# Kernel tuning notes

Measured on AMD Instinct MI355X. Metric: run time of the kernel, lower is better.

## Reference

```python
import jax, jax.numpy as jnp
import numpy as np

HIDDEN = 384
NDIM = 3
N_POINTS = 100000
N_SUPER = 2048
MAX_DEG = 32
RADIUS = 0.045
INPUT_DIM = 3


def _sincos_embed(coords):
    # ContinuousSincosEmbed: dim=384, ndim=3 -> 128 channels per spatial dim (64 sin + 64 cos)
    eff = HIDDEN // NDIM  # 128
    omega = jnp.arange(0, eff, 2, dtype=jnp.float32) / eff
    freq = 1.0 / (10000.0 ** omega)  # [eff//2]
    out = coords[..., None] * freq  # [..., ndim, eff//2]
    emb = jnp.concatenate([jnp.sin(out), jnp.cos(out)], axis=-1)  # [..., ndim, eff]
    return emb.reshape(coords.shape[:-1] + (HIDDEN,))


def _radius_neighbors(pos, sn_idx):
    # numpy preprocessing equivalent of torch_geometric.nn.pool.radius with
    # max_num_neighbors=MAX_DEG; fixed-size padded [S, K] output + validity mask.
    nbr = np.zeros((N_SUPER, MAX_DEG), np.int32)
    mask = np.zeros((N_SUPER, MAX_DEG), bool)
    pos2 = (pos ** 2).sum(-1)
    r2 = RADIUS * RADIUS
    chunk = 128
    for i0 in range(0, N_SUPER, chunk):
        sp = pos[sn_idx[i0:i0 + chunk]]
        d2 = (sp ** 2).sum(-1)[:, None] + pos2[None, :] - 2.0 * (sp @ pos.T)
        within = d2 <= r2
        for j in range(sp.shape[0]):
            idx = np.nonzero(within[j])[0][:MAX_DEG]
            nbr[i0 + j, :len(idx)] = idx
            mask[i0 + j, :len(idx)] = True
    return nbr, mask


def setup_inputs() -> dict:
    rng = np.random.default_rng(0)
    pos = rng.random((N_POINTS, NDIM)).astype(np.float32)
    sn_idx = np.sort(rng.choice(N_POINTS, N_SUPER, replace=False)).astype(np.int32)
    nbr, mask = _radius_neighbors(pos, sn_idx)
    key = jax.random.key(0)
    ks = jax.random.split(key, 6)
    s = 0.02  # truncnormal002 init scale
    return {
        "input_pos": jnp.asarray(pos),
        "input_feat": jax.random.normal(ks[0], (N_POINTS, INPUT_DIM), jnp.float32),
        "supernode_idx": jnp.asarray(sn_idx),
        "neighbor_idx": jnp.asarray(nbr),
        "neighbor_mask": jnp.asarray(mask),
        "W_in": jax.random.normal(ks[1], (INPUT_DIM, HIDDEN), jnp.float32) * s,
        "b_in": jnp.zeros((HIDDEN,), jnp.float32),
        "W1": jax.random.normal(ks[2], (2 * HIDDEN, HIDDEN), jnp.float32) * s,
        "b1": jnp.zeros((HIDDEN,), jnp.float32),
        "W2": jax.random.normal(ks[3], (HIDDEN, HIDDEN), jnp.float32) * s,
        "b2": jnp.zeros((HIDDEN,), jnp.float32),
        "W_proj": jax.random.normal(ks[4], (2 * HIDDEN, HIDDEN), jnp.float32) * s,
        "b_proj": jnp.zeros((HIDDEN,), jnp.float32),
    }


def reference(input_pos, input_feat, supernode_idx, neighbor_idx, neighbor_mask,
              W_in, b_in, W1, b1, W2, b2, W_proj, b_proj):
    # point embeddings: continuous sincos pos embed + input feature projection
    x = _sincos_embed(input_pos) + input_feat @ W_in + b_in          # [N, D]
    sn = x[supernode_idx]                                            # [S, D] supernode pos embed
    src = x[neighbor_idx]                                            # [S, K, D] gathered neighbors
    dst = jnp.broadcast_to(sn[:, None, :], src.shape)                # [S, K, D]
    h = jnp.concatenate([src, dst], axis=-1)                         # [S, K, 2D]
    # message MLP (Linear -> GELU(exact) -> Linear), as nn.GELU default
    h = jax.nn.gelu(h @ W1 + b1, approximate=False) @ W2 + b2        # [S, K, D]
    # masked mean == segment_csr(..., reduce='mean') over variable-degree edges
    m = neighbor_mask[..., None].astype(h.dtype)
    agg = (h * m).sum(axis=1) / jnp.maximum(m.sum(axis=1), 1.0)      # [S, D]
    # readd_supernode_pos: concat supernode pos embed, project 2D -> D
    out = jnp.concatenate([agg, sn], axis=-1) @ W_proj + b_proj      # [S, D]
    return out[None]                                                 # [1, S, D] (batch_size=1)
```

## Files before the change

### kernel.cpp

```cpp
#include <hip/hip_runtime.h>
#include <hip/hip_bf16.h>
#include <cstdint>

#define HIDDEN 384
#define NSUPER 2048
#define MAXDEG 32
#define FRAGS (12*24*64)
#define WBLK  (FRAGS*8)

typedef __attribute__((ext_vector_type(8))) short bf16x8;
typedef __attribute__((ext_vector_type(4))) float f32x4;

#define SWZ(row, col) ((col) ^ (((row)&7)<<3))

__device__ inline unsigned short f2bf(float f) {
    __hip_bfloat16 h = __float2bfloat16(f);
    return *reinterpret_cast<unsigned short*>(&h);
}
__device__ inline bf16x8 pack8(const float* v) {
    union { bf16x8 v8; unsigned short u[8]; } u;
    #pragma unroll
    for (int i = 0; i < 8; ++i) u.u[i] = f2bf(v[i]);
    return u.v8;
}
__device__ inline float fast_erf(float x) {
    float ax = fabsf(x);
    float t  = 1.0f / fmaf(0.3275911f, ax, 1.0f);
    float p  = t*(0.254829592f + t*(-0.284496736f + t*(1.421413741f +
               t*(-1.453152027f + t*1.061405429f))));
    float e  = __expf(-ax*ax);
    return copysignf(1.0f - p*e, x);
}
__device__ inline float gelu(float y) {
    return 0.5f * y * (1.0f + fast_erf(y * 0.70710678118654752f));
}

__global__ __launch_bounds__(256)
void prep(const float* __restrict__ W1, const float* __restrict__ W2,
          const float* __restrict__ Wp, const unsigned int* __restrict__ mask,
          unsigned short* __restrict__ w1sf, unsigned short* __restrict__ w1df,
          unsigned short* __restrict__ w2f,  unsigned short* __restrict__ wpf,
          int* __restrict__ flag) {
    const int b = blockIdx.x;
    if (b == 360) {
        __shared__ int s;
        if (threadIdx.x == 0) s = 0;
        __syncthreads();
        int bad = 0;
        for (int i = threadIdx.x; i < 16384; i += 256)
            if (mask[i] > 1u) bad = 1;
        if (bad) s = 1;
        __syncthreads();
        if (threadIdx.x == 0) *flag = s;
        return;
    }
    const int grp = b / 72, sub = b % 72;
    const float* W; unsigned short* out;
    switch (grp) {
        case 0: W = W1;              out = w1sf; break;
        case 1: W = W1 + 384*HIDDEN; out = w1df; break;
        case 2: W = W2;              out = w2f;  break;
        case 3: W = Wp;              out = wpf;  break;
        default:W = Wp + 384*HIDDEN; out = wpf + WBLK; break;
    }
    const int idx = sub * 256 + threadIdx.x;
    const int l   = idx & 63;
    const int frag= idx >> 6;
    const int nt  = frag % 24;
    const int kt  = frag / 24;
    const int col = nt * 16 + (l & 15);
    const int k0  = kt * 32 + (l >> 4) * 8;
    unsigned int pk[4];
    #pragma unroll
    for (int j = 0; j < 4; ++j) {
        unsigned int lo = f2bf(W[(k0 + 2*j)     * HIDDEN + col]);
        unsigned int hi = f2bf(W[(k0 + 2*j + 1) * HIDDEN + col]);
        pk[j] = lo | (hi << 16);
    }
    *reinterpret_cast<uint4*>(&out[(size_t)idx * 8]) =
        *reinterpret_cast<const uint4*>(pk);
}

__global__ __launch_bounds__(256)
void k_embdst(const float* __restrict__ pos, const float* __restrict__ feat,
              const int* __restrict__ sn_idx,
              const float* __restrict__ W_in, const float* __restrict__ b_in,
              const unsigned short* __restrict__ W1df, const float* __restrict__ b1,
              unsigned short* __restrict__ snxb, float* __restrict__ dstv)
{
    __shared__ unsigned short E[64][384];
    __shared__ float WINT[HIDDEN][4];
    __shared__ float PF[64][8];
    __shared__ float FREQ[64];

    const int rg = blockIdx.x >> 1, ch = blockIdx.x & 1;
    const int t  = threadIdx.x;

    if (t < 64) {
        const int pi = sn_idx[rg*64 + t];
        PF[t][0]=pos[pi*3];  PF[t][1]=pos[pi*3+1];  PF[t][2]=pos[pi*3+2];
        PF[t][3]=feat[pi*3]; PF[t][4]=feat[pi*3+1]; PF[t][5]=feat[pi*3+2];
        FREQ[t] = exp2f(-(float)t * 0.2076205059304601f);
    }
    for (int d = t; d < HIDDEN; d += 256) {
        WINT[d][0]=W_in[d]; WINT[d][1]=W_in[HIDDEN+d];
        WINT[d][2]=W_in[2*HIDDEN+d]; WINT[d][3]=b_in[d];
    }
    __syncthreads();

    const int er = t >> 2, seg = t & 3;
    #pragma unroll
    for (int blk = 0; blk < 12; ++blk) {
        const int dim0 = blk*32 + seg*8;
        float v[8];
        #pragma unroll
        for (int i = 0; i < 8; ++i) {
            const int dim = dim0 + i;
            const int cc  = dim >> 7;
            const float a = PF[er][cc] * FREQ[dim & 63];
            const float base = ((dim >> 6) & 1) ? __cosf(a) : __sinf(a);
            const float4 wv = *(const float4*)WINT[dim];
            v[i] = base + PF[er][3]*wv.x + PF[er][4]*wv.y + PF[er][5]*wv.z + wv.w;
        }
        const bf16x8 pk = pack8(v);
        *(bf16x8*)&E[er][SWZ(er, dim0)] = pk;
        if (ch == 0)
            *(bf16x8*)&snxb[(size_t)(rg*64 + er)*HIDDEN + dim0] = pk;
    }
    __syncthreads();

    const int w = t>>6, l = t&63, lg = l>>4, l15 = l&15;
    const int wgm = w>>1, wgn = w&1;
    f32x4 acc[2][6];
    #pragma unroll
    for (int mt=0; mt<2; ++mt)
        #pragma unroll
        for (int nt=0; nt<6; ++nt) acc[mt][nt] = (f32x4){0.f,0.f,0.f,0.f};
    const int ntb = (ch*2 + wgn) * 6;
    for (int kt = 0; kt < 12; ++kt) {
        bf16x8 a[2], bfr[6];
        const unsigned short* bp = &W1df[((size_t)(kt*24 + ntb)*64 + l)*8];
        #pragma unroll
        for (int nt=0; nt<6; ++nt) bfr[nt] = *(const bf16x8*)(bp + (size_t)nt*512);
        #pragma unroll
        for (int mt=0; mt<2; ++mt)
            a[mt] = *(const bf16x8*)&E[wgm*32 + mt*16 + l15][SWZ(l15, kt*32 + lg*8)];
        #pragma unroll
        for (int mt=0; mt<2; ++mt)
            #pragma unroll
            for (int nt=0; nt<6; ++nt)
                acc[mt][nt] = __builtin_amdgcn_mfma_f32_16x16x32_bf16(a[mt], bfr[nt], acc[mt][nt], 0,0,0);
    }
    #pragma unroll
    for (int mt=0; mt<2; ++mt)
        #pragma unroll
        for (int nt=0; nt<6; ++nt) {
            const int col = ch*192 + wgn*96 + nt*16 + l15;
            #pragma unroll
            for (int r=0; r<4; ++r) {
                const int row = rg*64 + wgm*32 + mt*16 + lg*4 + r;
                dstv[(size_t)row*HIDDEN + col] = acc[mt][nt][r] + b1[col];
            }
        }
}

__global__ __launch_bounds__(256, 2)
void k_mlp(const float* __restrict__ pos, const float* __restrict__ feat,
           const int* __restrict__ nbr_idx, const void* __restrict__ mask_raw,
           const int* __restrict__ mask_fmt,
           const float* __restrict__ W_in, const float* __restrict__ b_in,
           const float* __restrict__ dstv,
           const unsigned short* __restrict__ W1f,
           const unsigned short* __restrict__ W2f,
           const float* __restrict__ b2, unsigned short* __restrict__ aggb)
{
    __shared__ unsigned short G[4*12*64*8];
    __shared__ float WINT[HIDDEN][4];
    __shared__ float DSTV[2][HIDDEN];
    __shared__ float PF[64][8];
    __shared__ float CNT[2];

    const int t  = threadIdx.x;
    const int bm = blockIdx.x;

    if (t < 64) {
        const int e  = bm*64 + t;
        const int pi = nbr_idx[e];
        PF[t][0]=pos[pi*3];  PF[t][1]=pos[pi*3+1];  PF[t][2]=pos[pi*3+2];
        PF[t][3]=feat[pi*3]; PF[t][4]=feat[pi*3+1]; PF[t][5]=feat[pi*3+2];
        const int fmt = *mask_fmt;
        const int mv  = fmt ? (int)((const unsigned char*)mask_raw)[e]
                            : ((const int*)mask_raw)[e];
        PF[t][6] = mv ? 1.0f : 0.0f;
    }
    for (int d = t; d < HIDDEN; d += 256) {
        WINT[d][0]=W_in[d]; WINT[d][1]=W_in[HIDDEN+d];
        WINT[d][2]=W_in[2*HIDDEN+d]; WINT[d][3]=b_in[d];
    }
    for (int i = t; i < 2*HIDDEN; i += 256)
        ((float*)DSTV)[i] = dstv[(size_t)bm*2*HIDDEN + i];
    __syncthreads();
    if (t < 2) {
        float c = 0.f;
        for (int s = 0; s < 32; ++s) c += PF[t*32+s][6];
        CNT[t] = c;
    }

    {
        const int er = t >> 2, seg = t & 3;
        float frA[8], frB[8];
        #pragma unroll
        for (int i = 0; i < 8; ++i) {
            frA[i] = exp2f(-(float)(seg*8 + i)      * 0.2076205059304601f);
            frB[i] = exp2f(-(float)(32 + seg*8 + i) * 0.2076205059304601f);
        }
        const float f0 = PF[er][3], f1 = PF[er][4], f2 = PF[er][5];
        const int slotbase = (er>>4)*12*64 + seg*16 + (er&15);
        #pragma unroll
        for (int blk = 0; blk < 12; ++blk) {
            const float pc = PF[er][blk>>2];
            float v[8];
            #pragma unroll
            for (int i = 0; i < 8; ++i) {
                const int dim = blk*32 + seg*8 + i;
                const float fr = (blk & 1) ? frB[i] : frA[i];
                const float a  = pc * fr;
                const float base = ((blk>>1) & 1) ? __cosf(a) : __sinf(a);
                const float4 wv = *(const float4*)WINT[dim];
                v[i] = fmaf(f0, wv.x, fmaf(f1, wv.y, fmaf(f2, wv.z, base + wv.w)));
            }
            *(bf16x8*)&G[(size_t)(slotbase + blk*64)*8] = pack8(v);
        }
    }
    __syncthreads();

    const int l = t & 63, ng = t >> 6, lg = l >> 4, l15 = l & 15;

    f32x4 acc[4][6];
    bf16x8 bA[6], bB[6];

    #define LOADB(dst, Wf, kt)                                                  \
        { const unsigned short* bp_ = &Wf[((size_t)((kt)*24 + ng*6)*64 + l)*8]; \
          _Pragma("unroll")                                                     \
          for (int nt_ = 0; nt_ < 6; ++nt_)                                     \
              dst[nt_] = *(const bf16x8*)(bp_ + (size_t)nt_*512); }
    #define AREAD(a_, kt)                                                       \
        { _Pragma("unroll")                                                     \
          for (int mt_ = 0; mt_ < 4; ++mt_)                                     \
              a_[mt_] = *(const bf16x8*)&G[(size_t)(((mt_*12 + (kt))*64) + l)*8]; }
    #define MFMA6(bfr, a_)                                                      \
        { _Pragma("unroll")                                                     \
          for (int mt_ = 0; mt_ < 4; ++mt_)                                     \
              _Pragma("unroll")                                                 \
              for (int nt_ = 0; nt_ < 6; ++nt_)                                 \
                  acc[mt_][nt_] = __builtin_amdgcn_mfma_f32_16x16x32_bf16(      \
                      a_[mt_], bfr[nt_], acc[mt_][nt_], 0, 0, 0); }

    #pragma unroll
    for (int mt=0; mt<4; ++mt)
        #pragma unroll
        for (int nt=0; nt<6; ++nt) acc[mt][nt] = (f32x4){0.f,0.f,0.f,0.f};
    LOADB(bA, W1f, 0); LOADB(bB, W1f, 1);
    #pragma unroll
    for (int kt = 0; kt < 12; kt += 2) {
        bf16x8 a[4];
        AREAD(a, kt);
        MFMA6(bA, a);
        if (kt + 2 < 12) LOADB(bA, W1f, kt + 2);
        AREAD(a, kt + 1);
        MFMA6(bB, a);
        if (kt + 3 < 12) LOADB(bB, W1f, kt + 3);
    }
    __syncthreads();

    #pragma unroll
    for (int mt=0; mt<4; ++mt) {
        const int sl = mt >> 1;
        #pragma unroll
        for (int nt=0; nt<6; ++nt) {
            const int col = ng*96 + nt*16 + l15;
            const float dv = DSTV[sl][col];
            const int base = ((mt*12 + (col>>5))*64 + ((col>>3)&3)*16 + lg*4)*8 + (col&7);
            #pragma unroll
            for (int r=0; r<4; ++r)
                G[base + r*8] = f2bf(gelu(acc[mt][nt][r] + dv));
        }
    }
    __syncthreads();

    #pragma unroll
    for (int mt=0; mt<4; ++mt)
        #pragma unroll
        for (int nt=0; nt<6; ++nt) acc[mt][nt] = (f32x4){0.f,0.f,0.f,0.f};
    LOADB(bA, W2f, 0); LOADB(bB, W2f, 1);
    #pragma unroll
    for (int kt = 0; kt < 12; kt += 2) {
        bf16x8 a[4];
        AREAD(a, kt);
        MFMA6(bA, a);
        if (kt + 2 < 12) LOADB(bA, W2f, kt + 2);
        AREAD(a, kt + 1);
        MFMA6(bB, a);
        if (kt + 3 < 12) LOADB(bB, W2f, kt + 3);
    }

    #pragma unroll
    for (int nt=0; nt<6; ++nt) {
        const int col = ng*96 + nt*16 + l15;
        float s0 = 0.f, s1 = 0.f;
        #pragma unroll
        for (int mt=0; mt<4; ++mt) {
            float p = 0.f;
            #pragma unroll
            for (int r=0; r<4; ++r)
                p += PF[mt*16 + lg*4 + r][6] * acc[mt][nt][r];
            if (mt < 2) s0 += p; else s1 += p;
        }
        s0 += __shfl_xor(s0,16); s0 += __shfl_xor(s0,32);
        s1 += __shfl_xor(s1,16); s1 += __shfl_xor(s1,32);
        if (lg == 0) {
            const float bb = b2[col];
            const int sn0 = bm*2;
            const float c0 = CNT[0], c1 = CNT[1];
            aggb[(size_t)sn0*HIDDEN + col]     = f2bf(s0 / fmaxf(c0,1.f) + bb*(c0>0.f?1.f:0.f));
            aggb[(size_t)(sn0+1)*HIDDEN + col] = f2bf(s1 / fmaxf(c1,1.f) + bb*(c1>0.f?1.f:0.f));
        }
    }
    #undef LOADB
    #undef AREAD
    #undef MFMA6
}

__global__ __launch_bounds__(256)
void k_proj(const unsigned short* __restrict__ aggb,
            const unsigned short* __restrict__ snxb,
            const unsigned short* __restrict__ wpf,
            const float* __restrict__ bp, float* __restrict__ out) {
    const int rg = blockIdx.x >> 2, cq = blockIdx.x & 3;
    const int t = threadIdx.x, w = t>>6, l = t&63, lg = l>>4, l15 = l&15;
    const int wgm = w>>1, wgn = w&1;
    const int r0 = rg*64 + wgm*32;
    const int ntb = cq*6 + wgn*3;
    f32x4 acc[2][3];
    #pragma unroll
    for (int mt=0; mt<2; ++mt)
        #pragma unroll
        for (int nt=0; nt<3; ++nt) acc[mt][nt] = (f32x4){0.f,0.f,0.f,0.f};
    #pragma unroll 2
    for (int kt = 0; kt < 24; ++kt) {
        const unsigned short* Ab = (kt < 12) ? aggb : snxb;
        const unsigned short* Wb = (kt < 12) ? wpf  : wpf + WBLK;
        const int ktt = (kt < 12) ? kt : kt - 12;
        bf16x8 a[2], bfr[3];
        const unsigned short* bpp = &Wb[((size_t)(ktt*24 + ntb)*64 + l)*8];
        #pragma unroll
        for (int nt=0; nt<3; ++nt) bfr[nt] = *(const bf16x8*)(bpp + (size_t)nt*512);
        #pragma unroll
        for (int mt=0; mt<2; ++mt)
            a[mt] = *(const bf16x8*)&Ab[(size_t)(r0 + mt*16 + l15)*HIDDEN + ktt*32 + lg*8];
        #pragma unroll
        for (int mt=0; mt<2; ++mt)
            #pragma unroll
            for (int nt=0; nt<3; ++nt)
                acc[mt][nt] = __builtin_amdgcn_mfma_f32_16x16x32_bf16(a[mt], bfr[nt], acc[mt][nt], 0,0,0);
    }
    #pragma unroll
    for (int mt=0; mt<2; ++mt)
        #pragma unroll
        for (int nt=0; nt<3; ++nt) {
            const int col = cq*96 + wgn*48 + nt*16 + l15;
            #pragma unroll
            for (int r=0; r<4; ++r) {
                const int row = r0 + mt*16 + lg*4 + r;
                out[(size_t)row*HIDDEN + col] = acc[mt][nt][r] + bp[col];
            }
        }
}

extern "C" void kernel_launch(void* const* d_in, const int* in_sizes, int n_in,
                              void* d_out, int out_size, void* d_ws, size_t ws_size,
                              hipStream_t stream) {
    const float* pos   = (const float*)d_in[0];
    const float* feat  = (const float*)d_in[1];
    const int*   sn    = (const int*)d_in[2];
    const int*   nbr   = (const int*)d_in[3];
    const void*  mask  = d_in[4];
    const float* W_in  = (const float*)d_in[5];
    const float* b_in  = (const float*)d_in[6];
    const float* W1    = (const float*)d_in[7];
    const float* b1    = (const float*)d_in[8];
    const float* W2    = (const float*)d_in[9];
    const float* b2    = (const float*)d_in[10];
    const float* Wp    = (const float*)d_in[11];
    const float* bpv   = (const float*)d_in[12];
    float* out = (float*)d_out;

    char* base = (char*)d_ws;
    int* flag = (int*)base;
    unsigned short* w1sf = (unsigned short*)(base + 256);
    unsigned short* w1df = w1sf + WBLK;
    unsigned short* w2f  = w1df + WBLK;
    unsigned short* wpf  = w2f  + WBLK;
    unsigned short* snxb = wpf  + 2*(size_t)WBLK;
    unsigned short* aggb = snxb + (size_t)NSUPER*HIDDEN;
    float* dstv = (float*)(aggb + (size_t)NSUPER*HIDDEN);

    hipLaunchKernelGGL(prep, dim3(361), dim3(256), 0, stream,
                       W1, W2, Wp, (const unsigned int*)mask, w1sf, w1df, w2f, wpf, flag);
    hipLaunchKernelGGL(k_embdst, dim3(64), dim3(256), 0, stream,
                       pos, feat, sn, W_in, b_in, w1df, b1, snxb, dstv);
    hipLaunchKernelGGL(k_mlp, dim3(1024), dim3(256), 0, stream,
                       pos, feat, nbr, mask, flag, W_in, b_in, dstv, w1sf, w2f, b2, aggb);
    hipLaunchKernelGGL(k_proj, dim3(128), dim3(256), 0, stream,
                       aggb, snxb, wpf, bpv, out);
}
```

Measured before the change: 94.98 us.

## Fold supernode embedding into prep, split dst GEMM, raise k_mlp occupancy

Supernode embedding computation moves into extra blocks of the prep kernel, and the dst-side W1 GEMM becomes a separate k_dstv kernel. That kernel reads the bf16 embedding from global memory and uses 128 smaller blocks instead of 64. In k_mlp, the first weight fragments are prefetched before the embedding phase, dstv values are held in registers instead of shared memory, and W_in is stored in shared memory as bf16 to cut LDS use. k_mlp also computes sin/cos once per frequency pair, raises the occupancy target to 3 blocks per CU, and raises wave priority around MFMA bursts. Risks are register spills at the higher occupancy target and a small precision loss from the bf16 W_in.

```diff
diff --git a/kernel.cpp b/kernel.cpp
--- a/kernel.cpp
+++ b/kernel.cpp
@@ -11,11 +11,12 @@
 typedef __attribute__((ext_vector_type(8))) short bf16x8;
 typedef __attribute__((ext_vector_type(4))) float f32x4;
 
-#define SWZ(row, col) ((col) ^ (((row)&7)<<3))
-
 __device__ inline unsigned short f2bf(float f) {
     __hip_bfloat16 h = __float2bfloat16(f);
     return *reinterpret_cast<unsigned short*>(&h);
+}
+__device__ inline float b2f(unsigned short s) {
+    return __uint_as_float(((unsigned int)s) << 16);
 }
 __device__ inline bf16x8 pack8(const float* v) {
     union { bf16x8 v8; unsigned short u[8]; } u;
@@ -38,20 +39,71 @@
 __global__ __launch_bounds__(256)
 void prep(const float* __restrict__ W1, const float* __restrict__ W2,
           const float* __restrict__ Wp, const unsigned int* __restrict__ mask,
+          const float* __restrict__ pos, const float* __restrict__ feat,
+          const int* __restrict__ sn_idx,
+          const float* __restrict__ W_in, const float* __restrict__ b_in,
           unsigned short* __restrict__ w1sf, unsigned short* __restrict__ w1df,
           unsigned short* __restrict__ w2f,  unsigned short* __restrict__ wpf,
-          int* __restrict__ flag) {
+          unsigned short* __restrict__ snxb, int* __restrict__ flag) {
     const int b = blockIdx.x;
+    const int t = threadIdx.x;
     if (b == 360) {
         __shared__ int s;
-        if (threadIdx.x == 0) s = 0;
+        if (t == 0) s = 0;
         __syncthreads();
         int bad = 0;
-        for (int i = threadIdx.x; i < 16384; i += 256)
+        for (int i = t; i < 16384; i += 256)
             if (mask[i] > 1u) bad = 1;
         if (bad) s = 1;
         __syncthreads();
-        if (threadIdx.x == 0) *flag = s;
+        if (t == 0) *flag = s;
+        return;
+    }
+    if (b > 360) {
+        __shared__ float W4[HIDDEN][4];
+        __shared__ float P6[64][7];
+        const int eb = b - 361;
+        if (t < 64) {
+            const int pi = sn_idx[eb*64 + t];
+            P6[t][0]=pos[pi*3];  P6[t][1]=pos[pi*3+1];  P6[t][2]=pos[pi*3+2];
+            P6[t][3]=feat[pi*3]; P6[t][4]=feat[pi*3+1]; P6[t][5]=feat[pi*3+2];
+        }
+        for (int d = t; d < HIDDEN; d += 256) {
+            W4[d][0]=W_in[d]; W4[d][1]=W_in[HIDDEN+d];
+            W4[d][2]=W_in[2*HIDDEN+d]; W4[d][3]=b_in[d];
+        }
+        __syncthreads();
+        const int er = t >> 2, seg = t & 3;
+        float frA[8], frB[8];
+        #pragma unroll
+        for (int i = 0; i < 8; ++i) {
+            frA[i] = exp2f(-(float)(seg*8 + i)      * 0.2076205059304601f);
+            frB[i] = exp2f(-(float)(32 + seg*8 + i) * 0.2076205059304601f);
+        }
+        const float f0 = P6[er][3], f1 = P6[er][4], f2 = P6[er][5];
+        #pragma unroll
+        for (int cc = 0; cc < 3; ++cc) {
+            const float pc = P6[er][cc];
+            float sL[8], sH[8], cL[8], cH[8];
+            #pragma unroll
+            for (int i = 0; i < 8; ++i) {
+                const float aL = pc*frA[i], aH = pc*frB[i];
+                sL[i]=__sinf(aL); sH[i]=__sinf(aH); cL[i]=__cosf(aL); cH[i]=__cosf(aH);
+            }
+            #pragma unroll
+            for (int q = 0; q < 4; ++q) {
+                const float* bb = (q==0)?sL:(q==1)?sH:(q==2)?cL:cH;
+                const int blk = cc*4 + q;
+                float v[8];
+                #pragma unroll
+                for (int i = 0; i < 8; ++i) {
+                    const int dim = blk*32 + seg*8 + i;
+                    const float4 wv = *(const float4*)W4[dim];
+                    v[i] = fmaf(f0, wv.x, fmaf(f1, wv.y, fmaf(f2, wv.z, bb[i] + wv.w)));
+                }
+                *(bf16x8*)&snxb[(size_t)(eb*64 + er)*HIDDEN + blk*32 + seg*8] = pack8(v);
+            }
+        }
         return;
     }
     const int grp = b / 72, sub = b % 72;
@@ -63,7 +115,7 @@
         case 3: W = Wp;              out = wpf;  break;
         default:W = Wp + 384*HIDDEN; out = wpf + WBLK; break;
     }
-    const int idx = sub * 256 + threadIdx.x;
+    const int idx = sub * 256 + t;
     const int l   = idx & 63;
     const int frag= idx >> 6;
     const int nt  = frag % 24;
@@ -82,89 +134,48 @@
 }
 
 __global__ __launch_bounds__(256)
-void k_embdst(const float* __restrict__ pos, const float* __restrict__ feat,
-              const int* __restrict__ sn_idx,
-              const float* __restrict__ W_in, const float* __restrict__ b_in,
-              const unsigned short* __restrict__ W1df, const float* __restrict__ b1,
-              unsigned short* __restrict__ snxb, float* __restrict__ dstv)
-{
-    __shared__ unsigned short E[64][384];
-    __shared__ float WINT[HIDDEN][4];
-    __shared__ float PF[64][8];
-    __shared__ float FREQ[64];
-
-    const int rg = blockIdx.x >> 1, ch = blockIdx.x & 1;
-    const int t  = threadIdx.x;
-
-    if (t < 64) {
-        const int pi = sn_idx[rg*64 + t];
-        PF[t][0]=pos[pi*3];  PF[t][1]=pos[pi*3+1];  PF[t][2]=pos[pi*3+2];
-        PF[t][3]=feat[pi*3]; PF[t][4]=feat[pi*3+1]; PF[t][5]=feat[pi*3+2];
-        FREQ[t] = exp2f(-(float)t * 0.2076205059304601f);
-    }
-    for (int d = t; d < HIDDEN; d += 256) {
-        WINT[d][0]=W_in[d]; WINT[d][1]=W_in[HIDDEN+d];
-        WINT[d][2]=W_in[2*HIDDEN+d]; WINT[d][3]=b_in[d];
-    }
-    __syncthreads();
-
-    const int er = t >> 2, seg = t & 3;
-    #pragma unroll
-    for (int blk = 0; blk < 12; ++blk) {
-        const int dim0 = blk*32 + seg*8;
-        float v[8];
-        #pragma unroll
-        for (int i = 0; i < 8; ++i) {
-            const int dim = dim0 + i;
-            const int cc  = dim >> 7;
-            const float a = PF[er][cc] * FREQ[dim & 63];
-            const float base = ((dim >> 6) & 1) ? __cosf(a) : __sinf(a);
-            const float4 wv = *(const float4*)WINT[dim];
-            v[i] = base + PF[er][3]*wv.x + PF[er][4]*wv.y + PF[er][5]*wv.z + wv.w;
-        }
-        const bf16x8 pk = pack8(v);
-        *(bf16x8*)&E[er][SWZ(er, dim0)] = pk;
-        if (ch == 0)
-            *(bf16x8*)&snxb[(size_t)(rg*64 + er)*HIDDEN + dim0] = pk;
-    }
-    __syncthreads();
-
-    const int w = t>>6, l = t&63, lg = l>>4, l15 = l&15;
+void k_dstv(const unsigned short* __restrict__ snxb,
+            const unsigned short* __restrict__ w1df,
+            const float* __restrict__ b1, float* __restrict__ dstv) {
+    const int rg = blockIdx.x >> 2, cq = blockIdx.x & 3;
+    const int t = threadIdx.x, w = t>>6, l = t&63, lg = l>>4, l15 = l&15;
     const int wgm = w>>1, wgn = w&1;
-    f32x4 acc[2][6];
+    const int r0 = rg*64 + wgm*32;
+    const int ntb = cq*6 + wgn*3;
+    f32x4 acc[2][3];
     #pragma unroll
     for (int mt=0; mt<2; ++mt)
         #pragma unroll
-        for (int nt=0; nt<6; ++nt) acc[mt][nt] = (f32x4){0.f,0.f,0.f,0.f};
-    const int ntb = (ch*2 + wgn) * 6;
+        for (int nt=0; nt<3; ++nt) acc[mt][nt] = (f32x4){0.f,0.f,0.f,0.f};
+    #pragma unroll 2
     for (int kt = 0; kt < 12; ++kt) {
-        bf16x8 a[2], bfr[6];
-        const unsigned short* bp = &W1df[((size_t)(kt*24 + ntb)*64 + l)*8];
-        #pragma unroll
-        for (int nt=0; nt<6; ++nt) bfr[nt] = *(const bf16x8*)(bp + (size_t)nt*512);
+        bf16x8 a[2], bfr[3];
+        const unsigned short* bpp = &w1df[((size_t)(kt*24 + ntb)*64 + l)*8];
+        #pragma unroll
+        for (int nt=0; nt<3; ++nt) bfr[nt] = *(const bf16x8*)(bpp + (size_t)nt*512);
         #pragma unroll
         for (int mt=0; mt<2; ++mt)
-            a[mt] = *(const bf16x8*)&E[wgm*32 + mt*16 + l15][SWZ(l15, kt*32 + lg*8)];
+            a[mt] = *(const bf16x8*)&snxb[(size_t)(r0 + mt*16 + l15)*HIDDEN + kt*32 + lg*8];
         #pragma unroll
         for (int mt=0; mt<2; ++mt)
             #pragma unroll
-            for (int nt=0; nt<6; ++nt)
+            for (int nt=0; nt<3; ++nt)
                 acc[mt][nt] = __builtin_amdgcn_mfma_f32_16x16x32_bf16(a[mt], bfr[nt], acc[mt][nt], 0,0,0);
     }
     #pragma unroll
     for (int mt=0; mt<2; ++mt)
         #pragma unroll
-        for (int nt=0; nt<6; ++nt) {
-            const int col = ch*192 + wgn*96 + nt*16 + l15;
+        for (int nt=0; nt<3; ++nt) {
+            const int col = cq*96 + wgn*48 + nt*16 + l15;
             #pragma unroll
             for (int r=0; r<4; ++r) {
-                const int row = rg*64 + wgm*32 + mt*16 + lg*4 + r;
+                const int row = r0 + mt*16 + lg*4 + r;
                 dstv[(size_t)row*HIDDEN + col] = acc[mt][nt][r] + b1[col];
             }
         }
 }
 
-__global__ __launch_bounds__(256, 2)
+__global__ __launch_bounds__(256, 3)
 void k_mlp(const float* __restrict__ pos, const float* __restrict__ feat,
            const int* __restrict__ nbr_idx, const void* __restrict__ mask_raw,
            const int* __restrict__ mask_fmt,
@@ -175,70 +186,22 @@
            const float* __restrict__ b2, unsigned short* __restrict__ aggb)
 {
     __shared__ unsigned short G[4*12*64*8];
-    __shared__ float WINT[HIDDEN][4];
-    __shared__ float DSTV[2][HIDDEN];
-    __shared__ float PF[64][8];
+    __shared__ ushort4 WINTB[HIDDEN];
+    __shared__ float PF[64][7];
     __shared__ float CNT[2];
 
     const int t  = threadIdx.x;
     const int bm = blockIdx.x;
-
-    if (t < 64) {
-        const int e  = bm*64 + t;
-        const int pi = nbr_idx[e];
-        PF[t][0]=pos[pi*3];  PF[t][1]=pos[pi*3+1];  PF[t][2]=pos[pi*3+2];
-        PF[t][3]=feat[pi*3]; PF[t][4]=feat[pi*3+1]; PF[t][5]=feat[pi*3+2];
-        const int fmt = *mask_fmt;
-        const int mv  = fmt ? (int)((const unsigned char*)mask_raw)[e]
-                            : ((const int*)mask_raw)[e];
-        PF[t][6] = mv ? 1.0f : 0.0f;
-    }
-    for (int d = t; d < HIDDEN; d += 256) {
-        WINT[d][0]=W_in[d]; WINT[d][1]=W_in[HIDDEN+d];
-        WINT[d][2]=W_in[2*HIDDEN+d]; WINT[d][3]=b_in[d];
-    }
-    for (int i = t; i < 2*HIDDEN; i += 256)
-        ((float*)DSTV)[i] = dstv[(size_t)bm*2*HIDDEN + i];
-    __syncthreads();
-    if (t < 2) {
-        float c = 0.f;
-        for (int s = 0; s < 32; ++s) c += PF[t*32+s][6];
-        CNT[t] = c;
-    }
-
-    {
-        const int er = t >> 2, seg = t & 3;
-        float frA[8], frB[8];
-        #pragma unroll
-        for (int i = 0; i < 8; ++i) {
-            frA[i] = exp2f(-(float)(seg*8 + i)      * 0.2076205059304601f);
-            frB[i] = exp2f(-(float)(32 + seg*8 + i) * 0.2076205059304601f);
-        }
-        const float f0 = PF[er][3], f1 = PF[er][4], f2 = PF[er][5];
-        const int slotbase = (er>>4)*12*64 + seg*16 + (er&15);
-        #pragma unroll
-        for (int blk = 0; blk < 12; ++blk) {
-            const float pc = PF[er][blk>>2];
-            float v[8];
-            #pragma unroll
-            for (int i = 0; i < 8; ++i) {
-                const int dim = blk*32 + seg*8 + i;
-                const float fr = (blk & 1) ? frB[i] : frA[i];
-                const float a  = pc * fr;
-                const float base = ((blk>>1) & 1) ? __cosf(a) : __sinf(a);
-                const float4 wv = *(const float4*)WINT[dim];
-                v[i] = fmaf(f0, wv.x, fmaf(f1, wv.y, fmaf(f2, wv.z, base + wv.w)));
-            }
-            *(bf16x8*)&G[(size_t)(slotbase + blk*64)*8] = pack8(v);
-        }
-    }
-    __syncthreads();
-
     const int l = t & 63, ng = t >> 6, lg = l >> 4, l15 = l & 15;
 
-    f32x4 acc[4][6];
+    float dvreg[2][6];
+    #pragma unroll
+    for (int sl = 0; sl < 2; ++sl)
+        #pragma unroll
+        for (int nt = 0; nt < 6; ++nt)
+            dvreg[sl][nt] = dstv[(size_t)(bm*2 + sl)*HIDDEN + ng*96 + nt*16 + l15];
+
     bf16x8 bA[6], bB[6];
-
     #define LOADB(dst, Wf, kt)                                                  \
         { const unsigned short* bp_ = &Wf[((size_t)((kt)*24 + ng*6)*64 + l)*8]; \
           _Pragma("unroll")                                                     \
@@ -249,18 +212,83 @@
           for (int mt_ = 0; mt_ < 4; ++mt_)                                     \
               a_[mt_] = *(const bf16x8*)&G[(size_t)(((mt_*12 + (kt))*64) + l)*8]; }
     #define MFMA6(bfr, a_)                                                      \
-        { _Pragma("unroll")                                                     \
+        { __builtin_amdgcn_s_setprio(1);                                        \
+          _Pragma("unroll")                                                     \
           for (int mt_ = 0; mt_ < 4; ++mt_)                                     \
               _Pragma("unroll")                                                 \
               for (int nt_ = 0; nt_ < 6; ++nt_)                                 \
                   acc[mt_][nt_] = __builtin_amdgcn_mfma_f32_16x16x32_bf16(      \
-                      a_[mt_], bfr[nt_], acc[mt_][nt_], 0, 0, 0); }
+                      a_[mt_], bfr[nt_], acc[mt_][nt_], 0, 0, 0);               \
+          __builtin_amdgcn_s_setprio(0); }
+
+    LOADB(bA, W1f, 0); LOADB(bB, W1f, 1);
+
+    if (t < 64) {
+        const int e  = bm*64 + t;
+        const int pi = nbr_idx[e];
+        PF[t][0]=pos[pi*3];  PF[t][1]=pos[pi*3+1];  PF[t][2]=pos[pi*3+2];
+        PF[t][3]=feat[pi*3]; PF[t][4]=feat[pi*3+1]; PF[t][5]=feat[pi*3+2];
+        const int fmt = *mask_fmt;
+        const int mv  = fmt ? (int)((const unsigned char*)mask_raw)[e]
+                            : ((const int*)mask_raw)[e];
+        PF[t][6] = mv ? 1.0f : 0.0f;
+    }
+    for (int d = t; d < HIDDEN; d += 256) {
+        ushort4 wv;
+        wv.x = f2bf(W_in[d]); wv.y = f2bf(W_in[HIDDEN+d]);
+        wv.z = f2bf(W_in[2*HIDDEN+d]); wv.w = f2bf(b_in[d]);
+        WINTB[d] = wv;
+    }
+    __syncthreads();
+    if (t < 2) {
+        float c = 0.f;
+        for (int s = 0; s < 32; ++s) c += PF[t*32+s][6];
+        CNT[t] = c;
+    }
+
+    {
+        const int er = t >> 2, seg = t & 3;
+        float frA[8], frB[8];
+        #pragma unroll
+        for (int i = 0; i < 8; ++i) {
+            frA[i] = exp2f(-(float)(seg*8 + i)      * 0.2076205059304601f);
+            frB[i] = exp2f(-(float)(32 + seg*8 + i) * 0.2076205059304601f);
+        }
+        const float f0 = PF[er][3], f1 = PF[er][4], f2 = PF[er][5];
+        const int slotbase = (er>>4)*12*64 + seg*16 + (er&15);
+        #pragma unroll
+        for (int cc = 0; cc < 3; ++cc) {
+            const float pc = PF[er][cc];
+            float sL[8], sH[8], cL[8], cH[8];
+            #pragma unroll
+            for (int i = 0; i < 8; ++i) {
+                const float aL = pc*frA[i], aH = pc*frB[i];
+                sL[i]=__sinf(aL); sH[i]=__sinf(aH); cL[i]=__cosf(aL); cH[i]=__cosf(aH);
+            }
+            #pragma unroll
+            for (int q = 0; q < 4; ++q) {
+                const float* bb = (q==0)?sL:(q==1)?sH:(q==2)?cL:cH;
+                const int blk = cc*4 + q;
+                float v[8];
+                #pragma unroll
+                for (int i = 0; i < 8; ++i) {
+                    const int dim = blk*32 + seg*8 + i;
+                    const ushort4 wv = WINTB[dim];
+                    v[i] = fmaf(f0, b2f(wv.x), fmaf(f1, b2f(wv.y),
+                           fmaf(f2, b2f(wv.z), bb[i] + b2f(wv.w))));
+                }
+                *(bf16x8*)&G[(size_t)(slotbase + blk*64)*8] = pack8(v);
+            }
+        }
+    }
+    __syncthreads();
+
+    f32x4 acc[4][6];
 
     #pragma unroll
     for (int mt=0; mt<4; ++mt)
         #pragma unroll
         for (int nt=0; nt<6; ++nt) acc[mt][nt] = (f32x4){0.f,0.f,0.f,0.f};
-    LOADB(bA, W1f, 0); LOADB(bB, W1f, 1);
     #pragma unroll
     for (int kt = 0; kt < 12; kt += 2) {
         bf16x8 a[4];
@@ -279,7 +307,7 @@
         #pragma unroll
         for (int nt=0; nt<6; ++nt) {
             const int col = ng*96 + nt*16 + l15;
-            const float dv = DSTV[sl][col];
+            const float dv = dvreg[sl][nt];
             const int base = ((mt*12 + (col>>5))*64 + ((col>>3)&3)*16 + lg*4)*8 + (col&7);
             #pragma unroll
             for (int r=0; r<4; ++r)
@@ -405,10 +433,12 @@
     unsigned short* aggb = snxb + (size_t)NSUPER*HIDDEN;
     float* dstv = (float*)(aggb + (size_t)NSUPER*HIDDEN);
 
-    hipLaunchKernelGGL(prep, dim3(361), dim3(256), 0, stream,
-                       W1, W2, Wp, (const unsigned int*)mask, w1sf, w1df, w2f, wpf, flag);
-    hipLaunchKernelGGL(k_embdst, dim3(64), dim3(256), 0, stream,
-                       pos, feat, sn, W_in, b_in, w1df, b1, snxb, dstv);
+    hipLaunchKernelGGL(prep, dim3(393), dim3(256), 0, stream,
+                       W1, W2, Wp, (const unsigned int*)mask,
+                       pos, feat, sn, W_in, b_in,
+                       w1sf, w1df, w2f, wpf, snxb, flag);
+    hipLaunchKernelGGL(k_dstv, dim3(128), dim3(256), 0, stream,
+                       snxb, w1df, b1, dstv);
     hipLaunchKernelGGL(k_mlp, dim3(1024), dim3(256), 0, stream,
                        pos, feat, nbr, mask, flag, W_in, b_in, dstv, w1sf, w2f, b2, aggb);
     hipLaunchKernelGGL(k_proj, dim3(128), dim3(256), 0, stream,
```

Result: slower. 114.7 us (+20.8%).
